# Optimization experiments

Measured on AMD Instinct MI355X. Metric: run time of the kernel, lower is better.

## Reference

```python
import jax, jax.numpy as jnp
import numpy as np

FS = 44100.0
# Time-constant bounds (seconds) hard-coded from RC component values in __init__
T_AF_MIN, T_AF_MAX = 820.0 * 4.7e-07 * 0.8, 270000.0 * 4.7e-07 * 1.2
T_AS_MIN, T_AS_MAX = 820.0 * 6.8e-06 * 0.8, 270000.0 * 6.8e-06 * 100.0
T_SF_MIN, T_SF_MAX = 91000.0 * 4.7e-07 * 0.8, 1200000.0 * 4.7e-07 * 1.2
T_SS_MIN, T_SS_MAX = 750000.0 * 6.8e-06 * 0.8, 750000.0 * 6.8e-06 * 100.0


def _logit(p):
    p = min(max(p, 1e-06), 1.0 - 1e-06)
    return float(np.log(p / (1.0 - p)))


def _u_from_seconds(val_s, tmin, tmax):
    return _logit((val_s - tmin) / (tmax - tmin))


def setup_inputs() -> dict:
    key = jax.random.key(0)
    B, T = 128, 131072
    # dB-domain peak envelope, roughly -60..+10 dB so the -24 dB threshold is exercised
    x = jax.random.normal(key, (B, T), dtype=jnp.float32) * 12.0 - 18.0
    return {
        'x_peak_dB': x,
        'comp_thresh': jnp.float32(-24.0),
        'ratio_logit': jnp.float32(np.log(4.0 - 1.0)),
        'fb_logit': jnp.float32(_logit(0.5)),
        'u_T_af': jnp.float32(_u_from_seconds(0.01, T_AF_MIN, T_AF_MAX)),
        'u_T_as': jnp.float32(_u_from_seconds(0.05, T_AS_MIN, T_AS_MAX)),
        'u_T_sf': jnp.float32(_u_from_seconds(0.03, T_SF_MIN, T_SF_MAX)),
        'u_T_ss': jnp.float32(_u_from_seconds(0.2, T_SS_MIN, T_SS_MAX)),
    }


def _secs(u, tmin, tmax):
    return tmin + (tmax - tmin) * jax.nn.sigmoid(u)


def _ssl_comp_gain(x, comp_thresh, ratio_logit, fb_logit, u_T_af, u_T_as, u_T_sf, u_T_ss):
    # Parameter reparameterization (matches module.forward)
    cr = jnp.maximum(jnp.exp(ratio_logit) + 1.0, 1.0 + 1e-04)
    fb = jnp.clip(jax.nn.sigmoid(fb_logit), 0.0, 1.0)
    a_af = jnp.exp(-1.0 / (FS * _secs(u_T_af, T_AF_MIN, T_AF_MAX)))
    a_as = jnp.exp(-1.0 / (FS * _secs(u_T_as, T_AS_MIN, T_AS_MAX)))
    a_sf = jnp.exp(-1.0 / (FS * _secs(u_T_sf, T_SF_MIN, T_SF_MAX)))
    a_ss = jnp.exp(-1.0 / (FS * _secs(u_T_ss, T_SS_MIN, T_SS_MAX)))
    slope = 1.0 - 1.0 / cr

    B = x.shape[0]
    z = jnp.zeros((B,), x.dtype)

    def step(carry, x_t):
        ef, es, y_prev = carry  # fast/slow envelope states (dB reduction, >=0), prev gain (dB)
        lvl = x_t + fb * y_prev              # feedback sidechain level (dB)
        tgt = jnp.maximum(lvl - comp_thresh, 0.0) * slope  # target gain reduction (dB)
        e = 0.5 * (ef + es)
        att = tgt > e                        # hard gate: attack vs shunt (release)
        af = jnp.where(att, a_af, a_sf)
        as_ = jnp.where(att, a_as, a_ss)
        ef = af * ef + (1.0 - af) * tgt
        es = as_ * es + (1.0 - as_) * tgt
        y = -0.5 * (ef + es)                 # gain in dB (<= 0)
        return (ef, es, y), y

    _, ys = jax.lax.scan(step, (z, z, z), x.T)  # scan over time, x.T: (T, B)
    return ys.T  # (B, T)


def reference(x_peak_dB, comp_thresh, ratio_logit, fb_logit, u_T_af, u_T_as, u_T_sf, u_T_ss):
    return _ssl_comp_gain(x_peak_dB.astype(jnp.float32), comp_thresh, ratio_logit,
                          fb_logit, u_T_af, u_T_as, u_T_sf, u_T_ss)
```

## Files before the change

### kernel.cpp

```cpp
#include <hip/hip_runtime.h>
#include <hip/hip_fp16.h>
#include <math.h>


constexpr int   T_LEN    = 131072;
constexpr int   NCM      = 64;
constexpr int   CM       = T_LEN / NCM;
constexpr int   SUB      = 16;
constexpr int   NC       = NCM * SUB;
constexpr int   CF       = T_LEN / NC;
constexpr int   K        = 16;
constexpr float STEP_ES  = 8.0f / 15.0f;
constexpr float INV_STEP = 15.0f / 8.0f;
constexpr int   DPF      = 8;
constexpr int   NV_ROW   = T_LEN >> 2;
constexpr int   QROW     = T_LEN >> 2;
constexpr int   NIT      = 3;
constexpr int   LINK     = NCM * K;

__device__ void compute_params(
        float* __restrict__ pw,
        const float* cth, const float* rl, const float* fbl,
        const float* uaf, const float* uas, const float* usf, const float* uss)
{
    const double FS = 44100.0;
    const double T_AF_MIN = 820.0 * 4.7e-07 * 0.8,   T_AF_MAX = 270000.0 * 4.7e-07 * 1.2;
    const double T_AS_MIN = 820.0 * 6.8e-06 * 0.8,   T_AS_MAX = 270000.0 * 6.8e-06 * 100.0;
    const double T_SF_MIN = 91000.0 * 4.7e-07 * 0.8, T_SF_MAX = 1200000.0 * 4.7e-07 * 1.2;
    const double T_SS_MIN = 750000.0 * 6.8e-06 * 0.8, T_SS_MAX = 750000.0 * 6.8e-06 * 100.0;

    double cr    = fmax(exp((double)rl[0]) + 1.0, 1.0 + 1e-4);
    double fb    = 1.0 / (1.0 + exp(-(double)fbl[0]));
    double slope = 1.0 - 1.0 / cr;

    double s_af = T_AF_MIN + (T_AF_MAX - T_AF_MIN) / (1.0 + exp(-(double)uaf[0]));
    double s_as = T_AS_MIN + (T_AS_MAX - T_AS_MIN) / (1.0 + exp(-(double)uas[0]));
    double s_sf = T_SF_MIN + (T_SF_MAX - T_SF_MIN) / (1.0 + exp(-(double)usf[0]));
    double s_ss = T_SS_MIN + (T_SS_MAX - T_SS_MIN) / (1.0 + exp(-(double)uss[0]));

    float a_af = (float)exp(-1.0 / (FS * s_af));
    float a_as = (float)exp(-1.0 / (FS * s_as));
    float a_sf = (float)exp(-1.0 / (FS * s_sf));
    float a_ss = (float)exp(-1.0 / (FS * s_ss));
    double q = 0.5 * slope * fb;

    pw[0]  = (float)(-0.5 * slope);
    pw[1]  = (float)(0.5 * slope * (double)cth[0]);
    pw[2]  = (float)(-q);
    pw[3]  = (float)(0.5 + q);
    pw[4]  = a_af;  pw[5] = a_as;  pw[6] = a_sf;  pw[7] = a_ss;
    float e_af = a_af * a_af, e_as = a_as * a_as, e_sf = a_sf * a_sf, e_ss = a_ss * a_ss;
    pw[8]  = e_af * e_af;  pw[9]  = e_as * e_as;
    pw[10] = e_sf * e_sf;  pw[11] = e_ss * e_ss;
    pw[12] = (float)(-0.125 * slope);
}

__global__ __launch_bounds__(256) void ssl_tr(
        const float* __restrict__ x, float* __restrict__ xt,
        float* __restrict__ xq, float* __restrict__ pw,
        const float* cth, const float* rl, const float* fbl,
        const float* uaf, const float* uas, const float* usf, const float* uss)
{
    if (blockIdx.x == 0 && threadIdx.x == 0)
        compute_params(pw, cth, rl, fbl, uaf, uas, usf, uss);

    __shared__ float4 lds4[64][33];
    const int b    = blockIdx.x >> 4;
    const int tile = blockIdx.x & 15;
    const int tid  = threadIdx.x;
    const int c0   = tile * 64;

    const float4* __restrict__ x4 = reinterpret_cast<const float4*>(x) + (size_t)b * NV_ROW;
    float4* __restrict__ xt4      = reinterpret_cast<float4*>(xt) + (size_t)b * NV_ROW;
    float* __restrict__ xqr       = xq + (size_t)b * QROW;

    #pragma unroll
    for (int it = 0; it < 8; ++it) {
        int idx = it * 256 + tid;
        int c = idx >> 5, s4 = idx & 31;
        float4 v = x4[(size_t)(c0 + c) * 32 + s4];
        lds4[c][s4] = v;
        xqr[(size_t)(c0 + c) * 32 + s4] = (v.x + v.y) + (v.z + v.w);
    }
    __syncthreads();
    #pragma unroll
    for (int it = 0; it < 8; ++it) {
        int idx = it * 256 + tid;
        int blk = idx >> 6, c = idx & 63;
        xt4[(size_t)blk * 1024 + c0 + c] = lds4[c][blk];
    }
}

__global__ __launch_bounds__(256) void ssl_map_q(
        const float* __restrict__ xq, __half2* __restrict__ mp,
        const float* __restrict__ pw, int B)
{
    int tid = blockIdx.x * 256 + threadIdx.x;
    int k  = tid & (K - 1);
    int bc = tid >> 4;
    if (bc >= B * NCM) return;
    int c  = bc & (NCM - 1);
    int b  = bc >> 6;

    const float nhs_q = pw[12], hst = pw[1], nq = pw[2], r = pw[3];
    const float e_af = pw[8], e_as = pw[9], e_sf = pw[10], e_ss = pw[11];

    float v0s = -STEP_ES * (float)k;
    float EF = v0s, ES = v0s, Y = EF + ES;
    const float4* __restrict__ q4 =
        reinterpret_cast<const float4*>(xq) + (size_t)b * (QROW >> 2) + (size_t)c * (CM >> 4);

    float4 buf[DPF];
    #pragma unroll
    for (int i = 0; i < DPF; ++i) buf[i] = q4[i];

    #pragma unroll 1
    for (int s = 0; s < SUB; ++s) {
        #pragma unroll
        for (int i = 0; i < DPF; ++i) {
            float4 xv = buf[i];
            int nxt = s * DPF + DPF + i;
            if (nxt < (CM >> 4)) buf[i] = q4[nxt];
#define QSTEP(XS) { \
            float sx2 = fmaf(nhs_q, (XS), hst); \
            float u2  = fmaf(nq, Y, sx2); \
            float t2  = fminf(u2, 0.0f); \
            bool att  = sx2 < r * Y; \
            float af  = att ? e_af : e_sf; \
            float as2 = att ? e_as : e_ss; \
            EF = fmaf(af,  EF - t2, t2); \
            ES = fmaf(as2, ES - t2, t2); \
            Y  = EF + ES; }
            QSTEP(xv.x) QSTEP(xv.y) QSTEP(xv.z) QSTEP(xv.w)
#undef QSTEP
        }
        mp[((size_t)bc * SUB + s) * K + k] = __floats2half2_rn(EF, ES);
    }
}

__global__ __launch_bounds__(1024) void ssl_guess(
        const __half2* __restrict__ mp, float2* __restrict__ bnd,
        const float* __restrict__ pw, int B)
{
    __shared__ __half2 link_s[LINK];
    __shared__ float2 bnd_s[NC];
    const int b = blockIdx.x;
    const int t = threadIdx.x;

    {
        int c = t >> 4, k = t & 15;
        link_s[t] = mp[((size_t)(b * NCM + c) * SUB + (SUB - 1)) * K + k];
    }
    __syncthreads();

    if (t == 0) {
        float EF = 0.0f, ES = 0.0f;
        for (int c = 0; c < NCM; ++c) {
            bnd_s[SUB * c] = make_float2(EF, ES);
            float tt = -ES * INV_STEP;
            int idx = (int)tt;
            idx = idx < 0 ? 0 : (idx > K - 2 ? K - 2 : idx);
            float u = tt - (float)idx;
            float2 a0 = __half22float2(link_s[c * K + idx]);
            float2 a1 = __half22float2(link_s[c * K + idx + 1]);
            EF = a0.x + (a1.x - a0.x) * u;
            ES = a0.y + (a1.y - a0.y) * u;
        }
    }
    __syncthreads();
    {
        int c = t >> 4, j = t & 15;
        if (j > 0) {
            float ES = bnd_s[SUB * c].y;
            float tt = -ES * INV_STEP;
            int idx = (int)tt;
            idx = idx < 0 ? 0 : (idx > K - 2 ? K - 2 : idx);
            float u = tt - (float)idx;
            const __half2* m = mp + ((size_t)(b * NCM + c) * SUB + (j - 1)) * K;
            float2 a0 = __half22float2(m[idx]);
            float2 a1 = __half22float2(m[idx + 1]);
            bnd_s[t] = make_float2(a0.x + (a1.x - a0.x) * u,
                                   a0.y + (a1.y - a0.y) * u);
        }
    }
    __syncthreads();
    bnd[(size_t)b * NC + t] = bnd_s[t];
}

__global__ __launch_bounds__(256) void ssl_jac_g(
        const float* __restrict__ xt, const float2* __restrict__ bnd,
        float4* __restrict__ Jv, float2* __restrict__ gv,
        const float* __restrict__ pw)
{
    const int b = blockIdx.x >> 2;
    const int c = ((blockIdx.x & 3) << 8) | threadIdx.x;

    const float nhs = pw[0], hst = pw[1], nq = pw[2], r = pw[3];
    const float a_af = pw[4], a_as = pw[5], a_sf = pw[6], a_ss = pw[7];

    const float4* __restrict__ base4 =
        reinterpret_cast<const float4*>(xt) + (size_t)b * NV_ROW;

    float2 s0 = bnd[(size_t)b * NC + c];
    float EF = s0.x, ES = s0.y, Y = EF + ES;
    float jFx = 1.0f, jFy = 0.0f, jSx = 0.0f, jSy = 1.0f;

    float4 buf[DPF];
    #pragma unroll
    for (int i = 0; i < DPF; ++i) buf[i] = base4[(size_t)i * 1024 + c];

    #pragma unroll 1
    for (int vb = 0; vb < 32; vb += DPF) {
        #pragma unroll
        for (int i = 0; i < DPF; ++i) {
            float4 xv = buf[i];
            int nxt = vb + DPF + i;
            if (nxt < 32) buf[i] = base4[(size_t)nxt * 1024 + c];
#define SSL_STEP_J(XV) { \
            float sx2 = fmaf(nhs, (XV), hst); \
            float u2  = fmaf(nq, Y, sx2); \
            float t2  = fminf(u2, 0.0f); \
            float mm  = (u2 < 0.0f) ? nq : 0.0f; \
            bool att  = sx2 < r * Y; \
            float af  = att ? a_af : a_sf; \
            float as2 = att ? a_as : a_ss; \
            float jtx = mm * (jFx + jSx); \
            float jty = mm * (jFy + jSy); \
            jFx = fmaf(af,  jFx - jtx, jtx); \
            jFy = fmaf(af,  jFy - jty, jty); \
            jSx = fmaf(as2, jSx - jtx, jtx); \
            jSy = fmaf(as2, jSy - jty, jty); \
            EF  = fmaf(af,  EF - t2, t2); \
            ES  = fmaf(as2, ES - t2, t2); \
            Y   = EF + ES; }
            SSL_STEP_J(xv.x)
            SSL_STEP_J(xv.y)
            SSL_STEP_J(xv.z)
            SSL_STEP_J(xv.w)
#undef SSL_STEP_J
        }
    }
    Jv[(size_t)b * NC + c] = make_float4(jFx, jFy, jSx, jSy);
    gv[(size_t)b * NC + c] = make_float2(EF - (jFx * s0.x + jFy * s0.y),
                                         ES - (jSx * s0.x + jSy * s0.y));
}

__global__ __launch_bounds__(1024) void ssl_scan_g(
        const float4* __restrict__ Jv, const float2* __restrict__ gv,
        float2* __restrict__ bnd)
{
    __shared__ float4 aggJ[16];
    __shared__ float2 aggG[16];
    const int b = blockIdx.x;
    const int t = threadIdx.x;
    const int lane = t & 63, w = t >> 6;

    float4 J = Jv[(size_t)b * NC + t];
    float2 g = gv[(size_t)b * NC + t];
    float jFx = J.x, jFy = J.y, jSx = J.z, jSy = J.w, gx = g.x, gy = g.y;

    for (int d = 1; d < 64; d <<= 1) {
        float pa = __shfl_up(jFx, d), pb = __shfl_up(jFy, d);
        float pc = __shfl_up(jSx, d), pd = __shfl_up(jSy, d);
        float px = __shfl_up(gx, d),  py = __shfl_up(gy, d);
        if (lane >= d) {
            float na = jFx * pa + jFy * pc, nb = jFx * pb + jFy * pd;
            float nc = jSx * pa + jSy * pc, nd = jSx * pb + jSy * pd;
            gx = jFx * px + jFy * py + gx;
            gy = jSx * px + jSy * py + gy;
            jFx = na; jFy = nb; jSx = nc; jSy = nd;
        }
    }
    if (lane == 63) {
        aggJ[w] = make_float4(jFx, jFy, jSx, jSy);
        aggG[w] = make_float2(gx, gy);
    }
    __syncthreads();
    if (t < 16) {
        float4 Ja = aggJ[t]; float2 ga = aggG[t];
        float a = Ja.x, bb = Ja.y, c = Ja.z, dd = Ja.w, ggx = ga.x, ggy = ga.y;
        for (int d = 1; d < 16; d <<= 1) {
            float pa = __shfl_up(a, d), pb = __shfl_up(bb, d);
            float pc = __shfl_up(c, d), pd = __shfl_up(dd, d);
            float px = __shfl_up(ggx, d), py = __shfl_up(ggy, d);
            if (t >= d) {
                float na = a * pa + bb * pc, nb = a * pb + bb * pd;
                float nc = c * pa + dd * pc, nd = c * pb + dd * pd;
                ggx = a * px + bb * py + ggx;
                ggy = c * px + dd * py + ggy;
                a = na; bb = nb; c = nc; dd = nd;
            }
        }
        aggJ[t] = make_float4(a, bb, c, dd);
        aggG[t] = make_float2(ggx, ggy);
    }
    __syncthreads();
    float2 send;
    if (w == 0) send = make_float2(gx, gy);
    else {
        float2 pg = aggG[w - 1];
        send = make_float2(jFx * pg.x + jFy * pg.y + gx,
                           jSx * pg.x + jSy * pg.y + gy);
    }
    if (t < NC - 1) bnd[(size_t)b * NC + t + 1] = send;
    else            bnd[(size_t)b * NC] = make_float2(0.0f, 0.0f);
}

__global__ __launch_bounds__(256) void ssl_out_g(
        const float* __restrict__ xt, float* __restrict__ out,
        const float2* __restrict__ bnd, const float* __restrict__ pw)
{
    const int b = blockIdx.x >> 2;
    const int c = ((blockIdx.x & 3) << 8) | threadIdx.x;

    const float nhs = pw[0], hst = pw[1], nq = pw[2], r = pw[3];
    const float a_af = pw[4], a_as = pw[5], a_sf = pw[6], a_ss = pw[7];

    const float4* __restrict__ base4 =
        reinterpret_cast<const float4*>(xt) + (size_t)b * NV_ROW;
    float4* __restrict__ yr = reinterpret_cast<float4*>(out) + (size_t)b * NV_ROW;

    float2 s = bnd[(size_t)b * NC + c];
    float EF = s.x, ES = s.y, Y = EF + ES;

    float4 buf[DPF];
    #pragma unroll
    for (int i = 0; i < DPF; ++i) buf[i] = base4[(size_t)i * 1024 + c];

    #pragma unroll 1
    for (int vb = 0; vb < 32; vb += DPF) {
        #pragma unroll
        for (int i = 0; i < DPF; ++i) {
            float4 xv = buf[i];
            int nxt = vb + DPF + i;
            if (nxt < 32) buf[i] = base4[(size_t)nxt * 1024 + c];
            float4 yo;
#define SSL_STEP(XV, YOUT) { \
            float sx2 = fmaf(nhs, (XV), hst); \
            float u2  = fmaf(nq, Y, sx2); \
            float t2  = fminf(u2, 0.0f); \
            bool att  = sx2 < r * Y; \
            float af  = att ? a_af : a_sf; \
            float as2 = att ? a_as : a_ss; \
            EF = fmaf(af,  EF - t2, t2); \
            ES = fmaf(as2, ES - t2, t2); \
            Y  = EF + ES; \
            (YOUT) = Y; }
            SSL_STEP(xv.x, yo.x)
            SSL_STEP(xv.y, yo.y)
            SSL_STEP(xv.z, yo.z)
            SSL_STEP(xv.w, yo.w)
#undef SSL_STEP
            yr[(size_t)c * 32 + vb + i] = yo;
        }
    }
}

extern "C" void kernel_launch(void* const* d_in, const int* in_sizes, int n_in,
                              void* d_out, int out_size, void* d_ws, size_t ws_size,
                              hipStream_t stream) {
    const float* x = (const float*)d_in[0];
    const int B = in_sizes[0] / T_LEN;

    const size_t MP_B = (size_t)B * NCM * SUB * K * sizeof(__half2);
    const size_t PW_O = MP_B;
    const size_t XQ_O = PW_O + 256;
    const size_t XQ_B = (size_t)B * QROW * sizeof(float);
    const size_t XT_O = XQ_O + XQ_B;

    __half2* mp  = (__half2*)d_ws;
    float*   pw  = (float*)((char*)d_ws + PW_O);
    float*   xq  = (float*)((char*)d_ws + XQ_O);
    float*   xt  = (float*)((char*)d_ws + XT_O);
    float2*  bnd = (float2*)xq;
    float4*  Jv  = (float4*)((char*)xq + (1u << 20));
    float2*  gv  = (float2*)((char*)xq + (3u << 20));

    ssl_tr<<<16 * B, 256, 0, stream>>>(
        x, xt, xq, pw,
        (const float*)d_in[1], (const float*)d_in[2], (const float*)d_in[3],
        (const float*)d_in[4], (const float*)d_in[5], (const float*)d_in[6],
        (const float*)d_in[7]);

    int map_blocks = (B * NCM * K + 255) / 256;
    ssl_map_q<<<map_blocks, 256, 0, stream>>>(xq, mp, pw, B);

    ssl_guess<<<B, 1024, 0, stream>>>(mp, bnd, pw, B);

    for (int it = 0; it < NIT; ++it) {
        ssl_jac_g<<<4 * B, 256, 0, stream>>>(xt, bnd, Jv, gv, pw);
        ssl_scan_g<<<B, 1024, 0, stream>>>(Jv, gv, bnd);
    }

    ssl_out_g<<<4 * B, 256, 0, stream>>>(xt, (float*)d_out, bnd, pw);
}
```

Measured before the change: 156.0 us.

## Fuse Jacobian pass with cross-block scan via decoupled lookback flags

Merges the per-chunk Jacobian kernel and the separate per-row scan kernel into one kernel. Blocks publish their affine aggregates with release flags, and later blocks in the same row spin on them to get their prefix. The final iteration also computes the output directly from its own scanned state, so the separate output kernel is dropped. This removes four launches and the Jv/gv round trips through global memory, and the last iteration no longer re-reads the input a separate time. The cost is spin-waiting that relies on earlier blocks in a row being scheduled first, plus flags that must be zeroed each call.

```diff
diff --git a/kernel.cpp b/kernel.cpp
--- a/kernel.cpp
+++ b/kernel.cpp
@@ -58,11 +58,15 @@
 __global__ __launch_bounds__(256) void ssl_tr(
         const float* __restrict__ x, float* __restrict__ xt,
         float* __restrict__ xq, float* __restrict__ pw,
+        unsigned* __restrict__ flg, int nflg,
         const float* cth, const float* rl, const float* fbl,
         const float* uaf, const float* uas, const float* usf, const float* uss)
 {
-    if (blockIdx.x == 0 && threadIdx.x == 0)
-        compute_params(pw, cth, rl, fbl, uaf, uas, usf, uss);
+    if (blockIdx.x == 0) {
+        if (threadIdx.x == 0)
+            compute_params(pw, cth, rl, fbl, uaf, uas, usf, uss);
+        for (int i = threadIdx.x; i < nflg; i += 256) flg[i] = 0u;
+    }
 
     __shared__ float4 lds4[64][33];
     const int b    = blockIdx.x >> 4;
@@ -187,13 +191,22 @@
     bnd[(size_t)b * NC + t] = bnd_s[t];
 }
 
-__global__ __launch_bounds__(256) void ssl_jac_g(
-        const float* __restrict__ xt, const float2* __restrict__ bnd,
-        float4* __restrict__ Jv, float2* __restrict__ gv,
+template<bool LAST>
+__global__ __launch_bounds__(256) void ssl_js(
+        const float* __restrict__ xt,
+        const float2* __restrict__ bnd_in, float2* __restrict__ bnd_out,
+        float* __restrict__ out,
+        float* __restrict__ aJx, float* __restrict__ aJy,
+        float* __restrict__ aJz, float* __restrict__ aJw,
+        float* __restrict__ aGx, float* __restrict__ aGy,
+        unsigned* __restrict__ flg,
         const float* __restrict__ pw)
 {
-    const int b = blockIdx.x >> 2;
-    const int c = ((blockIdx.x & 3) << 8) | threadIdx.x;
+    const int blk = blockIdx.x;
+    const int b = blk >> 2, j = blk & 3;
+    const int tid = threadIdx.x;
+    const int c = (j << 8) | tid;
+    const int lane = tid & 63, w = tid >> 6;
 
     const float nhs = pw[0], hst = pw[1], nq = pw[2], r = pw[3];
     const float a_af = pw[4], a_as = pw[5], a_sf = pw[6], a_ss = pw[7];
@@ -201,7 +214,7 @@
     const float4* __restrict__ base4 =
         reinterpret_cast<const float4*>(xt) + (size_t)b * NV_ROW;
 
-    float2 s0 = bnd[(size_t)b * NC + c];
+    float2 s0 = bnd_in[(size_t)b * NC + c];
     float EF = s0.x, ES = s0.y, Y = EF + ES;
     float jFx = 1.0f, jFy = 0.0f, jSx = 0.0f, jSy = 1.0f;
 
@@ -240,24 +253,8 @@
 #undef SSL_STEP_J
         }
     }
-    Jv[(size_t)b * NC + c] = make_float4(jFx, jFy, jSx, jSy);
-    gv[(size_t)b * NC + c] = make_float2(EF - (jFx * s0.x + jFy * s0.y),
-                                         ES - (jSx * s0.x + jSy * s0.y));
-}
-
-__global__ __launch_bounds__(1024) void ssl_scan_g(
-        const float4* __restrict__ Jv, const float2* __restrict__ gv,
-        float2* __restrict__ bnd)
-{
-    __shared__ float4 aggJ[16];
-    __shared__ float2 aggG[16];
-    const int b = blockIdx.x;
-    const int t = threadIdx.x;
-    const int lane = t & 63, w = t >> 6;
-
-    float4 J = Jv[(size_t)b * NC + t];
-    float2 g = gv[(size_t)b * NC + t];
-    float jFx = J.x, jFy = J.y, jSx = J.z, jSy = J.w, gx = g.x, gy = g.y;
+    float gx = EF - (jFx * s0.x + jFy * s0.y);
+    float gy = ES - (jSx * s0.x + jSy * s0.y);
 
     for (int d = 1; d < 64; d <<= 1) {
         float pa = __shfl_up(jFx, d), pb = __shfl_up(jFy, d);
@@ -271,87 +268,107 @@
             jFx = na; jFy = nb; jSx = nc; jSy = nd;
         }
     }
-    if (lane == 63) {
-        aggJ[w] = make_float4(jFx, jFy, jSx, jSy);
-        aggG[w] = make_float2(gx, gy);
-    }
-    __syncthreads();
-    if (t < 16) {
-        float4 Ja = aggJ[t]; float2 ga = aggG[t];
-        float a = Ja.x, bb = Ja.y, c = Ja.z, dd = Ja.w, ggx = ga.x, ggy = ga.y;
-        for (int d = 1; d < 16; d <<= 1) {
-            float pa = __shfl_up(a, d), pb = __shfl_up(bb, d);
-            float pc = __shfl_up(c, d), pd = __shfl_up(dd, d);
-            float px = __shfl_up(ggx, d), py = __shfl_up(ggy, d);
-            if (t >= d) {
-                float na = a * pa + bb * pc, nb = a * pb + bb * pd;
-                float nc = c * pa + dd * pc, nd = c * pb + dd * pd;
-                ggx = a * px + bb * py + ggx;
-                ggy = c * px + dd * py + ggy;
-                a = na; bb = nb; c = nc; dd = nd;
+
+    __shared__ float4 wJ[4];  __shared__ float2 wG[4];
+    __shared__ float4 pJ[3];  __shared__ float2 pG[3];
+    if (lane == 63) { wJ[w] = make_float4(jFx, jFy, jSx, jSy); wG[w] = make_float2(gx, gy); }
+    __syncthreads();
+
+    if (tid == 0) {
+        float4 A = wJ[0]; float2 ag = wG[0];
+        #pragma unroll
+        for (int q = 1; q < 4; ++q) {
+            float4 Bq = wJ[q]; float2 bg = wG[q];
+            float nx = Bq.x * A.x + Bq.y * A.z, ny = Bq.x * A.y + Bq.y * A.w;
+            float nz = Bq.z * A.x + Bq.w * A.z, nw = Bq.z * A.y + Bq.w * A.w;
+            float ngx = Bq.x * ag.x + Bq.y * ag.y + bg.x;
+            float ngy = Bq.z * ag.x + Bq.w * ag.y + bg.y;
+            A = make_float4(nx, ny, nz, nw); ag = make_float2(ngx, ngy);
+        }
+        __hip_atomic_store(&aJx[blk], A.x,  __ATOMIC_RELAXED, __HIP_MEMORY_SCOPE_AGENT);
+        __hip_atomic_store(&aJy[blk], A.y,  __ATOMIC_RELAXED, __HIP_MEMORY_SCOPE_AGENT);
+        __hip_atomic_store(&aJz[blk], A.z,  __ATOMIC_RELAXED, __HIP_MEMORY_SCOPE_AGENT);
+        __hip_atomic_store(&aJw[blk], A.w,  __ATOMIC_RELAXED, __HIP_MEMORY_SCOPE_AGENT);
+        __hip_atomic_store(&aGx[blk], ag.x, __ATOMIC_RELAXED, __HIP_MEMORY_SCOPE_AGENT);
+        __hip_atomic_store(&aGy[blk], ag.y, __ATOMIC_RELAXED, __HIP_MEMORY_SCOPE_AGENT);
+        __hip_atomic_store(&flg[blk], 1u,   __ATOMIC_RELEASE, __HIP_MEMORY_SCOPE_AGENT);
+    }
+
+    if (tid < j) {
+        int p = (b << 2) + tid;
+        while (__hip_atomic_load(&flg[p], __ATOMIC_ACQUIRE, __HIP_MEMORY_SCOPE_AGENT) == 0u) {}
+        pJ[tid] = make_float4(
+            __hip_atomic_load(&aJx[p], __ATOMIC_RELAXED, __HIP_MEMORY_SCOPE_AGENT),
+            __hip_atomic_load(&aJy[p], __ATOMIC_RELAXED, __HIP_MEMORY_SCOPE_AGENT),
+            __hip_atomic_load(&aJz[p], __ATOMIC_RELAXED, __HIP_MEMORY_SCOPE_AGENT),
+            __hip_atomic_load(&aJw[p], __ATOMIC_RELAXED, __HIP_MEMORY_SCOPE_AGENT));
+        pG[tid] = make_float2(
+            __hip_atomic_load(&aGx[p], __ATOMIC_RELAXED, __HIP_MEMORY_SCOPE_AGENT),
+            __hip_atomic_load(&aGy[p], __ATOMIC_RELAXED, __HIP_MEMORY_SCOPE_AGENT));
+    }
+    __syncthreads();
+
+    float2 v = make_float2(0.0f, 0.0f);
+    for (int p = 0; p < j; ++p) {
+        float4 A = pJ[p]; float2 g2 = pG[p];
+        v = make_float2(A.x * v.x + A.y * v.y + g2.x,
+                        A.z * v.x + A.w * v.y + g2.y);
+    }
+    for (int q = 0; q < w; ++q) {
+        float4 A = wJ[q]; float2 g2 = wG[q];
+        v = make_float2(A.x * v.x + A.y * v.y + g2.x,
+                        A.z * v.x + A.w * v.y + g2.y);
+    }
+
+    if (!LAST) {
+        float ux = jFx * v.x + jFy * v.y + gx;
+        float uy = jSx * v.x + jSy * v.y + gy;
+        if (c < NC - 1) bnd_out[(size_t)b * NC + c + 1] = make_float2(ux, uy);
+        if (c == 0)     bnd_out[(size_t)b * NC] = make_float2(0.0f, 0.0f);
+    } else {
+        float pa = __shfl_up(jFx, 1), pb = __shfl_up(jFy, 1);
+        float pc = __shfl_up(jSx, 1), pd = __shfl_up(jSy, 1);
+        float px = __shfl_up(gx, 1),  py = __shfl_up(gy, 1);
+        float sx, sy;
+        if (lane == 0) { sx = v.x; sy = v.y; }
+        else {
+            sx = pa * v.x + pb * v.y + px;
+            sy = pc * v.x + pd * v.y + py;
+        }
+
+        float EFo = sx, ESo = sy, Yo = EFo + ESo;
+        float4* __restrict__ yr = reinterpret_cast<float4*>(out) + (size_t)b * NV_ROW;
+
+        float4 bufo[DPF];
+        #pragma unroll
+        for (int i = 0; i < DPF; ++i) bufo[i] = base4[(size_t)i * 1024 + c];
+
+        #pragma unroll 1
+        for (int vb = 0; vb < 32; vb += DPF) {
+            #pragma unroll
+            for (int i = 0; i < DPF; ++i) {
+                float4 xv = bufo[i];
+                int nxt = vb + DPF + i;
+                if (nxt < 32) bufo[i] = base4[(size_t)nxt * 1024 + c];
+                float4 yo;
+#define SSL_STEP(XV, YOUT) { \
+                float sx2 = fmaf(nhs, (XV), hst); \
+                float u2  = fmaf(nq, Yo, sx2); \
+                float t2  = fminf(u2, 0.0f); \
+                bool att  = sx2 < r * Yo; \
+                float af  = att ? a_af : a_sf; \
+                float as2 = att ? a_as : a_ss; \
+                EFo = fmaf(af,  EFo - t2, t2); \
+                ESo = fmaf(as2, ESo - t2, t2); \
+                Yo  = EFo + ESo; \
+                (YOUT) = Yo; }
+                SSL_STEP(xv.x, yo.x)
+                SSL_STEP(xv.y, yo.y)
+                SSL_STEP(xv.z, yo.z)
+                SSL_STEP(xv.w, yo.w)
+#undef SSL_STEP
+                yr[(size_t)c * 32 + vb + i] = yo;
             }
-        }
-        aggJ[t] = make_float4(a, bb, c, dd);
-        aggG[t] = make_float2(ggx, ggy);
-    }
-    __syncthreads();
-    float2 send;
-    if (w == 0) send = make_float2(gx, gy);
-    else {
-        float2 pg = aggG[w - 1];
-        send = make_float2(jFx * pg.x + jFy * pg.y + gx,
-                           jSx * pg.x + jSy * pg.y + gy);
-    }
-    if (t < NC - 1) bnd[(size_t)b * NC + t + 1] = send;
-    else            bnd[(size_t)b * NC] = make_float2(0.0f, 0.0f);
-}
-
-__global__ __launch_bounds__(256) void ssl_out_g(
-        const float* __restrict__ xt, float* __restrict__ out,
-        const float2* __restrict__ bnd, const float* __restrict__ pw)
-{
-    const int b = blockIdx.x >> 2;
-    const int c = ((blockIdx.x & 3) << 8) | threadIdx.x;
-
-    const float nhs = pw[0], hst = pw[1], nq = pw[2], r = pw[3];
-    const float a_af = pw[4], a_as = pw[5], a_sf = pw[6], a_ss = pw[7];
-
-    const float4* __restrict__ base4 =
-        reinterpret_cast<const float4*>(xt) + (size_t)b * NV_ROW;
-    float4* __restrict__ yr = reinterpret_cast<float4*>(out) + (size_t)b * NV_ROW;
-
-    float2 s = bnd[(size_t)b * NC + c];
-    float EF = s.x, ES = s.y, Y = EF + ES;
-
-    float4 buf[DPF];
-    #pragma unroll
-    for (int i = 0; i < DPF; ++i) buf[i] = base4[(size_t)i * 1024 + c];
-
-    #pragma unroll 1
-    for (int vb = 0; vb < 32; vb += DPF) {
-        #pragma unroll
-        for (int i = 0; i < DPF; ++i) {
-            float4 xv = buf[i];
-            int nxt = vb + DPF + i;
-            if (nxt < 32) buf[i] = base4[(size_t)nxt * 1024 + c];
-            float4 yo;
-#define SSL_STEP(XV, YOUT) { \
-            float sx2 = fmaf(nhs, (XV), hst); \
-            float u2  = fmaf(nq, Y, sx2); \
-            float t2  = fminf(u2, 0.0f); \
-            bool att  = sx2 < r * Y; \
-            float af  = att ? a_af : a_sf; \
-            float as2 = att ? a_as : a_ss; \
-            EF = fmaf(af,  EF - t2, t2); \
-            ES = fmaf(as2, ES - t2, t2); \
-            Y  = EF + ES; \
-            (YOUT) = Y; }
-            SSL_STEP(xv.x, yo.x)
-            SSL_STEP(xv.y, yo.y)
-            SSL_STEP(xv.z, yo.z)
-            SSL_STEP(xv.w, yo.w)
-#undef SSL_STEP
-            yr[(size_t)c * 32 + vb + i] = yo;
         }
     }
 }
@@ -361,23 +378,33 @@
                               hipStream_t stream) {
     const float* x = (const float*)d_in[0];
     const int B = in_sizes[0] / T_LEN;
-
-    const size_t MP_B = (size_t)B * NCM * SUB * K * sizeof(__half2);
-    const size_t PW_O = MP_B;
-    const size_t XQ_O = PW_O + 256;
-    const size_t XQ_B = (size_t)B * QROW * sizeof(float);
-    const size_t XT_O = XQ_O + XQ_B;
+    const int NBLK = 4 * B;
+
+    const size_t MP_B  = (size_t)B * NCM * SUB * K * sizeof(__half2);
+    const size_t PW_O  = MP_B;
+    const size_t AT_O  = PW_O + 1024;
+    const size_t AT_SZ = (size_t)NBLK * NIT * sizeof(float);
+    const size_t XQ_O  = AT_O + 7 * ((AT_SZ + 255) & ~255ull) + 256;
+    const size_t XQ_B  = (size_t)B * QROW * sizeof(float);
+    const size_t XT_O  = XQ_O + XQ_B;
 
     __half2* mp  = (__half2*)d_ws;
     float*   pw  = (float*)((char*)d_ws + PW_O);
+    const size_t AT_STRIDE = (AT_SZ + 255) & ~255ull;
+    float* aJx = (float*)((char*)d_ws + AT_O + 0 * AT_STRIDE);
+    float* aJy = (float*)((char*)d_ws + AT_O + 1 * AT_STRIDE);
+    float* aJz = (float*)((char*)d_ws + AT_O + 2 * AT_STRIDE);
+    float* aJw = (float*)((char*)d_ws + AT_O + 3 * AT_STRIDE);
+    float* aGx = (float*)((char*)d_ws + AT_O + 4 * AT_STRIDE);
+    float* aGy = (float*)((char*)d_ws + AT_O + 5 * AT_STRIDE);
+    unsigned* flg = (unsigned*)((char*)d_ws + AT_O + 6 * AT_STRIDE);
     float*   xq  = (float*)((char*)d_ws + XQ_O);
     float*   xt  = (float*)((char*)d_ws + XT_O);
-    float2*  bnd = (float2*)xq;
-    float4*  Jv  = (float4*)((char*)xq + (1u << 20));
-    float2*  gv  = (float2*)((char*)xq + (3u << 20));
+    float2*  bndA = (float2*)xq;
+    float2*  bndB = bndA + (size_t)B * NC;
 
     ssl_tr<<<16 * B, 256, 0, stream>>>(
-        x, xt, xq, pw,
+        x, xt, xq, pw, flg, NBLK * NIT,
         (const float*)d_in[1], (const float*)d_in[2], (const float*)d_in[3],
         (const float*)d_in[4], (const float*)d_in[5], (const float*)d_in[6],
         (const float*)d_in[7]);
@@ -385,12 +412,18 @@
     int map_blocks = (B * NCM * K + 255) / 256;
     ssl_map_q<<<map_blocks, 256, 0, stream>>>(xq, mp, pw, B);
 
-    ssl_guess<<<B, 1024, 0, stream>>>(mp, bnd, pw, B);
-
-    for (int it = 0; it < NIT; ++it) {
-        ssl_jac_g<<<4 * B, 256, 0, stream>>>(xt, bnd, Jv, gv, pw);
-        ssl_scan_g<<<B, 1024, 0, stream>>>(Jv, gv, bnd);
-    }
-
-    ssl_out_g<<<4 * B, 256, 0, stream>>>(xt, (float*)d_out, bnd, pw);
-}
+    ssl_guess<<<B, 1024, 0, stream>>>(mp, bndA, pw, B);
+
+    ssl_js<false><<<NBLK, 256, 0, stream>>>(
+        xt, bndA, bndB, nullptr,
+        aJx + 0 * NBLK, aJy + 0 * NBLK, aJz + 0 * NBLK, aJw + 0 * NBLK,
+        aGx + 0 * NBLK, aGy + 0 * NBLK, flg + 0 * NBLK, pw);
+    ssl_js<false><<<NBLK, 256, 0, stream>>>(
+        xt, bndB, bndA, nullptr,
+        aJx + 1 * NBLK, aJy + 1 * NBLK, aJz + 1 * NBLK, aJw + 1 * NBLK,
+        aGx + 1 * NBLK, aGy + 1 * NBLK, flg + 1 * NBLK, pw);
+    ssl_js<true><<<NBLK, 256, 0, stream>>>(
+        xt, bndA, nullptr, (float*)d_out,
+        aJx + 2 * NBLK, aJy + 2 * NBLK, aJz + 2 * NBLK, aJw + 2 * NBLK,
+        aGx + 2 * NBLK, aGy + 2 * NBLK, flg + 2 * NBLK, pw);
+}
```

New measurement: 182.8 us. +17.1%, slower.

## Fuse affine boundary scan into Jacobian and output kernels, dropping scan launches

Applied to the files above, without the earlier changes.

Each of the four 256-thread blocks of a row now redoes the full 1024-chunk affine prefix scan of the previous iteration's Jacobians in shared memory, so the separate ssl_scan_g kernel is no longer needed. Each thread first composes four consecutive chunk maps, then a wave-level shuffle scan and a serial pass over the wave totals give the boundary states. This removes three kernel launches and the round-trip of boundary states through global memory, and Jacobian buffers are ping-ponged between iterations. The cost is that every block repeats the scan redundantly and reads four times more J/g data.

```diff
diff --git a/kernel.cpp b/kernel.cpp
--- a/kernel.cpp
+++ b/kernel.cpp
@@ -15,7 +15,6 @@
 constexpr int   DPF      = 8;
 constexpr int   NV_ROW   = T_LEN >> 2;
 constexpr int   QROW     = T_LEN >> 2;
-constexpr int   NIT      = 3;
 constexpr int   LINK     = NCM * K;
 
 __device__ void compute_params(
@@ -53,6 +52,16 @@
     pw[8]  = e_af * e_af;  pw[9]  = e_as * e_as;
     pw[10] = e_sf * e_sf;  pw[11] = e_ss * e_ss;
     pw[12] = (float)(-0.125 * slope);
+}
+
+__device__ __forceinline__ void aff_compose(float4& A, float2& g,
+                                            const float4 Bq, const float2 bg)
+{
+    float nx = Bq.x * A.x + Bq.y * A.z, ny = Bq.x * A.y + Bq.y * A.w;
+    float nz = Bq.z * A.x + Bq.w * A.z, nw = Bq.z * A.y + Bq.w * A.w;
+    float ngx = Bq.x * g.x + Bq.y * g.y + bg.x;
+    float ngy = Bq.z * g.x + Bq.w * g.y + bg.y;
+    A = make_float4(nx, ny, nz, nw); g = make_float2(ngx, ngy);
 }
 
 __global__ __launch_bounds__(256) void ssl_tr(
@@ -187,13 +196,20 @@
     bnd[(size_t)b * NC + t] = bnd_s[t];
 }
 
-__global__ __launch_bounds__(256) void ssl_jac_g(
-        const float* __restrict__ xt, const float2* __restrict__ bnd,
-        float4* __restrict__ Jv, float2* __restrict__ gv,
+template<int MODE>
+__global__ __launch_bounds__(256) void ssl_js(
+        const float* __restrict__ xt,
+        const float2* __restrict__ bnd0,
+        const float4* __restrict__ Jin, const float2* __restrict__ gin,
+        float4* __restrict__ Jout, float2* __restrict__ gout,
+        float* __restrict__ out,
         const float* __restrict__ pw)
 {
-    const int b = blockIdx.x >> 2;
-    const int c = ((blockIdx.x & 3) << 8) | threadIdx.x;
+    const int blk = blockIdx.x;
+    const int b = blk >> 2, j = blk & 3;
+    const int tid = threadIdx.x;
+    const int c = (j << 8) | tid;
+    const int lane = tid & 63, w = tid >> 6;
 
     const float nhs = pw[0], hst = pw[1], nq = pw[2], r = pw[3];
     const float a_af = pw[4], a_as = pw[5], a_sf = pw[6], a_ss = pw[7];
@@ -201,157 +217,141 @@
     const float4* __restrict__ base4 =
         reinterpret_cast<const float4*>(xt) + (size_t)b * NV_ROW;
 
-    float2 s0 = bnd[(size_t)b * NC + c];
-    float EF = s0.x, ES = s0.y, Y = EF + ES;
-    float jFx = 1.0f, jFy = 0.0f, jSx = 0.0f, jSy = 1.0f;
-
-    float4 buf[DPF];
-    #pragma unroll
-    for (int i = 0; i < DPF; ++i) buf[i] = base4[(size_t)i * 1024 + c];
-
-    #pragma unroll 1
-    for (int vb = 0; vb < 32; vb += DPF) {
+    __shared__ float2 bnd_s[NC];
+    __shared__ float4 wWJ[4];
+    __shared__ float2 wWG[4];
+
+    if (MODE >= 1) {
+        const float4* Jr = Jin + (size_t)b * NC;
+        const float2* gr = gin + (size_t)b * NC;
+        float4 J0 = Jr[4 * tid + 0], J1 = Jr[4 * tid + 1],
+               J2 = Jr[4 * tid + 2], J3 = Jr[4 * tid + 3];
+        float2 g0 = gr[4 * tid + 0], g1 = gr[4 * tid + 1],
+               g2 = gr[4 * tid + 2], g3 = gr[4 * tid + 3];
+
+        float4 A = J0; float2 ag = g0;
+        aff_compose(A, ag, J1, g1);
+        aff_compose(A, ag, J2, g2);
+        aff_compose(A, ag, J3, g3);
+
+        float jFx = A.x, jFy = A.y, jSx = A.z, jSy = A.w, gx = ag.x, gy = ag.y;
+        for (int d = 1; d < 64; d <<= 1) {
+            float pa = __shfl_up(jFx, d), pb = __shfl_up(jFy, d);
+            float pc = __shfl_up(jSx, d), pd = __shfl_up(jSy, d);
+            float px = __shfl_up(gx, d),  py = __shfl_up(gy, d);
+            if (lane >= d) {
+                float na = jFx * pa + jFy * pc, nb = jFx * pb + jFy * pd;
+                float nc = jSx * pa + jSy * pc, nd = jSx * pb + jSy * pd;
+                gx = jFx * px + jFy * py + gx;
+                gy = jSx * px + jSy * py + gy;
+                jFx = na; jFy = nb; jSx = nc; jSy = nd;
+            }
+        }
+        if (lane == 63) { wWJ[w] = make_float4(jFx, jFy, jSx, jSy); wWG[w] = make_float2(gx, gy); }
+        __syncthreads();
+
+        float2 v0 = make_float2(0.0f, 0.0f);
+        for (int q = 0; q < w; ++q) {
+            float4 Wq = wWJ[q]; float2 Wg = wWG[q];
+            v0 = make_float2(Wq.x * v0.x + Wq.y * v0.y + Wg.x,
+                             Wq.z * v0.x + Wq.w * v0.y + Wg.y);
+        }
+        float pa = __shfl_up(jFx, 1), pb = __shfl_up(jFy, 1);
+        float pc = __shfl_up(jSx, 1), pd = __shfl_up(jSy, 1);
+        float px = __shfl_up(gx, 1),  py = __shfl_up(gy, 1);
+        float2 v;
+        if (lane == 0) v = v0;
+        else v = make_float2(pa * v0.x + pb * v0.y + px,
+                             pc * v0.x + pd * v0.y + py);
+
+        bnd_s[4 * tid + 0] = v;
+        v = make_float2(J0.x * v.x + J0.y * v.y + g0.x, J0.z * v.x + J0.w * v.y + g0.y);
+        bnd_s[4 * tid + 1] = v;
+        v = make_float2(J1.x * v.x + J1.y * v.y + g1.x, J1.z * v.x + J1.w * v.y + g1.y);
+        bnd_s[4 * tid + 2] = v;
+        v = make_float2(J2.x * v.x + J2.y * v.y + g2.x, J2.z * v.x + J2.w * v.y + g2.y);
+        bnd_s[4 * tid + 3] = v;
+        __syncthreads();
+    }
+
+    float2 s0 = (MODE == 0) ? bnd0[(size_t)b * NC + c] : bnd_s[c];
+
+    if (MODE <= 1) {
+        float EF = s0.x, ES = s0.y, Y = EF + ES;
+        float jFx = 1.0f, jFy = 0.0f, jSx = 0.0f, jSy = 1.0f;
+
+        float4 buf[DPF];
         #pragma unroll
-        for (int i = 0; i < DPF; ++i) {
-            float4 xv = buf[i];
-            int nxt = vb + DPF + i;
-            if (nxt < 32) buf[i] = base4[(size_t)nxt * 1024 + c];
+        for (int i = 0; i < DPF; ++i) buf[i] = base4[(size_t)i * 1024 + c];
+
+        #pragma unroll 1
+        for (int vb = 0; vb < 32; vb += DPF) {
+            #pragma unroll
+            for (int i = 0; i < DPF; ++i) {
+                float4 xv = buf[i];
+                int nxt = vb + DPF + i;
+                if (nxt < 32) buf[i] = base4[(size_t)nxt * 1024 + c];
 #define SSL_STEP_J(XV) { \
-            float sx2 = fmaf(nhs, (XV), hst); \
-            float u2  = fmaf(nq, Y, sx2); \
-            float t2  = fminf(u2, 0.0f); \
-            float mm  = (u2 < 0.0f) ? nq : 0.0f; \
-            bool att  = sx2 < r * Y; \
-            float af  = att ? a_af : a_sf; \
-            float as2 = att ? a_as : a_ss; \
-            float jtx = mm * (jFx + jSx); \
-            float jty = mm * (jFy + jSy); \
-            jFx = fmaf(af,  jFx - jtx, jtx); \
-            jFy = fmaf(af,  jFy - jty, jty); \
-            jSx = fmaf(as2, jSx - jtx, jtx); \
-            jSy = fmaf(as2, jSy - jty, jty); \
-            EF  = fmaf(af,  EF - t2, t2); \
-            ES  = fmaf(as2, ES - t2, t2); \
-            Y   = EF + ES; }
-            SSL_STEP_J(xv.x)
-            SSL_STEP_J(xv.y)
-            SSL_STEP_J(xv.z)
-            SSL_STEP_J(xv.w)
+                float sx2 = fmaf(nhs, (XV), hst); \
+                float u2  = fmaf(nq, Y, sx2); \
+                float t2  = fminf(u2, 0.0f); \
+                float mm  = (u2 < 0.0f) ? nq : 0.0f; \
+                bool att  = sx2 < r * Y; \
+                float af  = att ? a_af : a_sf; \
+                float as2 = att ? a_as : a_ss; \
+                float jtx = mm * (jFx + jSx); \
+                float jty = mm * (jFy + jSy); \
+                jFx = fmaf(af,  jFx - jtx, jtx); \
+                jFy = fmaf(af,  jFy - jty, jty); \
+                jSx = fmaf(as2, jSx - jtx, jtx); \
+                jSy = fmaf(as2, jSy - jty, jty); \
+                EF  = fmaf(af,  EF - t2, t2); \
+                ES  = fmaf(as2, ES - t2, t2); \
+                Y   = EF + ES; }
+                SSL_STEP_J(xv.x)
+                SSL_STEP_J(xv.y)
+                SSL_STEP_J(xv.z)
+                SSL_STEP_J(xv.w)
 #undef SSL_STEP_J
-        }
-    }
-    Jv[(size_t)b * NC + c] = make_float4(jFx, jFy, jSx, jSy);
-    gv[(size_t)b * NC + c] = make_float2(EF - (jFx * s0.x + jFy * s0.y),
-                                         ES - (jSx * s0.x + jSy * s0.y));
-}
-
-__global__ __launch_bounds__(1024) void ssl_scan_g(
-        const float4* __restrict__ Jv, const float2* __restrict__ gv,
-        float2* __restrict__ bnd)
-{
-    __shared__ float4 aggJ[16];
-    __shared__ float2 aggG[16];
-    const int b = blockIdx.x;
-    const int t = threadIdx.x;
-    const int lane = t & 63, w = t >> 6;
-
-    float4 J = Jv[(size_t)b * NC + t];
-    float2 g = gv[(size_t)b * NC + t];
-    float jFx = J.x, jFy = J.y, jSx = J.z, jSy = J.w, gx = g.x, gy = g.y;
-
-    for (int d = 1; d < 64; d <<= 1) {
-        float pa = __shfl_up(jFx, d), pb = __shfl_up(jFy, d);
-        float pc = __shfl_up(jSx, d), pd = __shfl_up(jSy, d);
-        float px = __shfl_up(gx, d),  py = __shfl_up(gy, d);
-        if (lane >= d) {
-            float na = jFx * pa + jFy * pc, nb = jFx * pb + jFy * pd;
-            float nc = jSx * pa + jSy * pc, nd = jSx * pb + jSy * pd;
-            gx = jFx * px + jFy * py + gx;
-            gy = jSx * px + jSy * py + gy;
-            jFx = na; jFy = nb; jSx = nc; jSy = nd;
-        }
-    }
-    if (lane == 63) {
-        aggJ[w] = make_float4(jFx, jFy, jSx, jSy);
-        aggG[w] = make_float2(gx, gy);
-    }
-    __syncthreads();
-    if (t < 16) {
-        float4 Ja = aggJ[t]; float2 ga = aggG[t];
-        float a = Ja.x, bb = Ja.y, c = Ja.z, dd = Ja.w, ggx = ga.x, ggy = ga.y;
-        for (int d = 1; d < 16; d <<= 1) {
-            float pa = __shfl_up(a, d), pb = __shfl_up(bb, d);
-            float pc = __shfl_up(c, d), pd = __shfl_up(dd, d);
-            float px = __shfl_up(ggx, d), py = __shfl_up(ggy, d);
-            if (t >= d) {
-                float na = a * pa + bb * pc, nb = a * pb + bb * pd;
-                float nc = c * pa + dd * pc, nd = c * pb + dd * pd;
-                ggx = a * px + bb * py + ggx;
-                ggy = c * px + dd * py + ggy;
-                a = na; bb = nb; c = nc; dd = nd;
             }
         }
-        aggJ[t] = make_float4(a, bb, c, dd);
-        aggG[t] = make_float2(ggx, ggy);
-    }
-    __syncthreads();
-    float2 send;
-    if (w == 0) send = make_float2(gx, gy);
-    else {
-        float2 pg = aggG[w - 1];
-        send = make_float2(jFx * pg.x + jFy * pg.y + gx,
-                           jSx * pg.x + jSy * pg.y + gy);
-    }
-    if (t < NC - 1) bnd[(size_t)b * NC + t + 1] = send;
-    else            bnd[(size_t)b * NC] = make_float2(0.0f, 0.0f);
-}
-
-__global__ __launch_bounds__(256) void ssl_out_g(
-        const float* __restrict__ xt, float* __restrict__ out,
-        const float2* __restrict__ bnd, const float* __restrict__ pw)
-{
-    const int b = blockIdx.x >> 2;
-    const int c = ((blockIdx.x & 3) << 8) | threadIdx.x;
-
-    const float nhs = pw[0], hst = pw[1], nq = pw[2], r = pw[3];
-    const float a_af = pw[4], a_as = pw[5], a_sf = pw[6], a_ss = pw[7];
-
-    const float4* __restrict__ base4 =
-        reinterpret_cast<const float4*>(xt) + (size_t)b * NV_ROW;
-    float4* __restrict__ yr = reinterpret_cast<float4*>(out) + (size_t)b * NV_ROW;
-
-    float2 s = bnd[(size_t)b * NC + c];
-    float EF = s.x, ES = s.y, Y = EF + ES;
-
-    float4 buf[DPF];
-    #pragma unroll
-    for (int i = 0; i < DPF; ++i) buf[i] = base4[(size_t)i * 1024 + c];
-
-    #pragma unroll 1
-    for (int vb = 0; vb < 32; vb += DPF) {
+        Jout[(size_t)b * NC + c] = make_float4(jFx, jFy, jSx, jSy);
+        gout[(size_t)b * NC + c] = make_float2(EF - (jFx * s0.x + jFy * s0.y),
+                                               ES - (jSx * s0.x + jSy * s0.y));
+    } else {
+        float EF = s0.x, ES = s0.y, Y = EF + ES;
+        float4* __restrict__ yr = reinterpret_cast<float4*>(out) + (size_t)b * NV_ROW;
+
+        float4 buf[DPF];
         #pragma unroll
-        for (int i = 0; i < DPF; ++i) {
-            float4 xv = buf[i];
-            int nxt = vb + DPF + i;
-            if (nxt < 32) buf[i] = base4[(size_t)nxt * 1024 + c];
-            float4 yo;
+        for (int i = 0; i < DPF; ++i) buf[i] = base4[(size_t)i * 1024 + c];
+
+        #pragma unroll 1
+        for (int vb = 0; vb < 32; vb += DPF) {
+            #pragma unroll
+            for (int i = 0; i < DPF; ++i) {
+                float4 xv = buf[i];
+                int nxt = vb + DPF + i;
+                if (nxt < 32) buf[i] = base4[(size_t)nxt * 1024 + c];
+                float4 yo;
 #define SSL_STEP(XV, YOUT) { \
-            float sx2 = fmaf(nhs, (XV), hst); \
-            float u2  = fmaf(nq, Y, sx2); \
-            float t2  = fminf(u2, 0.0f); \
-            bool att  = sx2 < r * Y; \
-            float af  = att ? a_af : a_sf; \
-            float as2 = att ? a_as : a_ss; \
-            EF = fmaf(af,  EF - t2, t2); \
-            ES = fmaf(as2, ES - t2, t2); \
-            Y  = EF + ES; \
-            (YOUT) = Y; }
-            SSL_STEP(xv.x, yo.x)
-            SSL_STEP(xv.y, yo.y)
-            SSL_STEP(xv.z, yo.z)
-            SSL_STEP(xv.w, yo.w)
+                float sx2 = fmaf(nhs, (XV), hst); \
+                float u2  = fmaf(nq, Y, sx2); \
+                float t2  = fminf(u2, 0.0f); \
+                bool att  = sx2 < r * Y; \
+                float af  = att ? a_af : a_sf; \
+                float as2 = att ? a_as : a_ss; \
+                EF = fmaf(af,  EF - t2, t2); \
+                ES = fmaf(as2, ES - t2, t2); \
+                Y  = EF + ES; \
+                (YOUT) = Y; }
+                SSL_STEP(xv.x, yo.x)
+                SSL_STEP(xv.y, yo.y)
+                SSL_STEP(xv.z, yo.z)
+                SSL_STEP(xv.w, yo.w)
 #undef SSL_STEP
-            yr[(size_t)c * 32 + vb + i] = yo;
+                yr[(size_t)c * 32 + vb + i] = yo;
+            }
         }
     }
 }
@@ -361,10 +361,11 @@
                               hipStream_t stream) {
     const float* x = (const float*)d_in[0];
     const int B = in_sizes[0] / T_LEN;
+    const size_t NCt = (size_t)B * NC;
 
     const size_t MP_B = (size_t)B * NCM * SUB * K * sizeof(__half2);
     const size_t PW_O = MP_B;
-    const size_t XQ_O = PW_O + 256;
+    const size_t XQ_O = PW_O + 1024;
     const size_t XQ_B = (size_t)B * QROW * sizeof(float);
     const size_t XT_O = XQ_O + XQ_B;
 
@@ -372,9 +373,12 @@
     float*   pw  = (float*)((char*)d_ws + PW_O);
     float*   xq  = (float*)((char*)d_ws + XQ_O);
     float*   xt  = (float*)((char*)d_ws + XT_O);
-    float2*  bnd = (float2*)xq;
-    float4*  Jv  = (float4*)((char*)xq + (1u << 20));
-    float2*  gv  = (float2*)((char*)xq + (3u << 20));
+
+    float2* bnd0 = (float2*)xq;
+    float4* JvA  = (float4*)(bnd0 + NCt);
+    float2* gvA  = (float2*)(JvA + NCt);
+    float4* JvB  = (float4*)(gvA + NCt);
+    float2* gvB  = (float2*)(JvB + NCt);
 
     ssl_tr<<<16 * B, 256, 0, stream>>>(
         x, xt, xq, pw,
@@ -385,12 +389,16 @@
     int map_blocks = (B * NCM * K + 255) / 256;
     ssl_map_q<<<map_blocks, 256, 0, stream>>>(xq, mp, pw, B);
 
-    ssl_guess<<<B, 1024, 0, stream>>>(mp, bnd, pw, B);
-
-    for (int it = 0; it < NIT; ++it) {
-        ssl_jac_g<<<4 * B, 256, 0, stream>>>(xt, bnd, Jv, gv, pw);
-        ssl_scan_g<<<B, 1024, 0, stream>>>(Jv, gv, bnd);
-    }
-
-    ssl_out_g<<<4 * B, 256, 0, stream>>>(xt, (float*)d_out, bnd, pw);
-}
+    ssl_guess<<<B, 1024, 0, stream>>>(mp, bnd0, pw, B);
+
+    const int NBLK = 4 * B;
+
+    ssl_js<0><<<NBLK, 256, 0, stream>>>(xt, bnd0, nullptr, nullptr,
+                                        JvA, gvA, nullptr, pw);
+    ssl_js<1><<<NBLK, 256, 0, stream>>>(xt, nullptr, JvA, gvA,
+                                        JvB, gvB, nullptr, pw);
+    ssl_js<1><<<NBLK, 256, 0, stream>>>(xt, nullptr, JvB, gvB,
+                                        JvA, gvA, nullptr, pw);
+    ssl_js<2><<<NBLK, 256, 0, stream>>>(xt, nullptr, JvA, gvA,
+                                        nullptr, nullptr, (float*)d_out, pw);
+}
```

Result: faster. 149.3 us (-4.3%).
